# Optimization experiments

Hardware: AMD Instinct MI355X
Metric: run time of the kernel (lower is better)

The kernel has to match this reference:

```python
import jax, jax.numpy as jnp
from jax import lax
import numpy as np

NBINS = 50

def _make_filters():
    coords = np.linspace(-1.0, 1.0, 3)
    zz, yy, xx = np.meshgrid(coords, coords, coords, indexing='ij')
    gf = []
    for freq in [2.0, 4.0]:
        for ang in [0.0, np.pi / 4, np.pi / 2, 3 * np.pi / 4]:
            gauss = np.exp(-(xx ** 2 + yy ** 2 + zz ** 2) / 0.5)
            f = gauss * np.cos(freq * (xx * np.cos(ang) + yy * np.sin(ang)))
            f = f - f.mean()
            s = f.std(ddof=1)  # torch std is unbiased
            if s > 1e-8:
                f = f / s
            gf.append(f)
    gf = np.stack(gf)[:, None].astype(np.float32)  # (8,1,3,3,3)
    lf = []
    for axis in range(3):
        for sign in [1, -1]:
            f = np.zeros((3, 3, 3), np.float32)
            f[1, 1, 1] = 1.0
            idx = [1, 1, 1]
            idx[axis] += sign
            f[tuple(idx)] = -1.0
            lf.append(f)
    lf = np.stack(lf)[:, None].astype(np.float32)  # (6,1,3,3,3)
    return gf, lf

def setup_inputs() -> dict:
    key = jax.random.key(0)
    k1, k2 = jax.random.split(key)
    B, D, H, W = 4, 96, 160, 160
    x = jax.random.uniform(k1, (B, 1, D, H, W), jnp.float32, minval=-1.0, maxval=1.0)
    mask = (jax.random.uniform(k2, (B, 1, D, H, W), jnp.float32) > 0.5).astype(jnp.float32)
    gf, lf = _make_filters()
    return {"x": x, "mask": mask, "gabor_filters": jnp.asarray(gf), "lbp_filters": jnp.asarray(lf)}

def _hu_stats(v, mf):
    # v, mf: (B,D,H,W); mf is 0/1 float mask
    n = mf.sum((1, 2, 3))                      # (B,)
    nn = jnp.maximum(n, 1.0)
    mu = (mf * v).sum((1, 2, 3)) / nn
    diff = (v - mu[:, None, None, None]) * mf
    var = (diff ** 2).sum((1, 2, 3)) / jnp.maximum(n - 1.0, 1.0)  # unbiased, like torch .std()
    sigma = jnp.sqrt(var) + 1e-8
    z = diff / sigma[:, None, None, None]
    skew = (z ** 3).sum((1, 2, 3)) / nn
    kurt = (z ** 4).sum((1, 2, 3)) / nn - 3.0
    # histogram over [-1,1] with 50 bins; torch.histc ignores out-of-range, last bin inclusive
    w = mf * ((v >= -1.0) & (v <= 1.0)).astype(v.dtype)
    idx = jnp.clip(jnp.floor((v + 1.0) * (NBINS / 2.0)).astype(jnp.int32), 0, NBINS - 1)
    hist = jax.vmap(lambda i, wb: jnp.zeros((NBINS,), v.dtype).at[i.ravel()].add(wb.ravel()))(idx, w)
    p = hist / (hist.sum(-1, keepdims=True) + 1e-8)
    ent = -(p * jnp.log(p + 1e-8)).sum(-1)
    valid = (n >= 10.0).astype(v.dtype)
    return jnp.stack([mu, sigma, skew, kurt, ent], axis=1) * valid[:, None]  # (B,5)

def _glcm_proxy(v, m):
    # v: (B,D,H,W) float; m: (B,D,H,W) bool
    rows = []
    for axis in range(3):
        a = axis + 1
        sl1 = tuple(slice(None, -1) if i == a else slice(None) for i in range(4))
        sl2 = tuple(slice(1, None) if i == a else slice(None) for i in range(4))
        d = v[sl1] - v[sl2]
        mp = (m[sl1] & m[sl2]).astype(v.dtype)
        s = mp.sum((1, 2, 3))
        ss = jnp.maximum(s, 1.0)
        con = (mp * d * d).sum((1, 2, 3)) / ss
        hom = (mp / (1.0 + d * d)).sum((1, 2, 3)) / ss
        ok = (s >= 4.0).astype(v.dtype)
        rows += [con * ok, hom * ok]
    return jnp.stack(rows, axis=1)  # (B,6)

def _forward(x, mask, gabor_filters, lbp_filters):
    v = x[:, 0]                       # (B,D,H,W)
    m = mask[:, 0] > 0.5              # bool
    mf = m.astype(x.dtype)
    hu = _hu_stats(v, mf)             # (B,5)
    dn = ('NCDHW', 'OIDHW', 'NCDHW')
    pad = [(1, 1)] * 3
    gab = lax.conv_general_dilated(x, gabor_filters, (1, 1, 1), pad, dimension_numbers=dn)
    lung_vol = jnp.clip(mask.sum((2, 3, 4)), 1.0, None)      # (B,1)
    gab_feat = jnp.abs(gab * mask).sum((2, 3, 4)) / lung_vol  # (B,8)
    lbp = lax.conv_general_dilated(x, lbp_filters, (1, 1, 1), pad, dimension_numbers=dn)
    lbp = lbp * mask
    lbp_feat = ((lbp > 0).astype(x.dtype) * mask).sum((2, 3, 4)) / lung_vol  # (B,6)
    glcm = _glcm_proxy(v, m)          # (B,6)
    return jnp.concatenate([hu, gab_feat, lbp_feat, glcm], axis=1)  # (B,25)

def reference(x, mask, gabor_filters, lbp_filters):
    return _forward(x, mask, gabor_filters, lbp_filters)
```

## Files before the change

### kernel.cpp

```cpp
#include <hip/hip_runtime.h>
#include <math.h>

#define B_    4
#define D_    96
#define H_    160
#define W_    160
#define HW_   (H_ * W_)
#define NVOX  (D_ * H_ * W_)
#define NBINS 50
#define NQ    78
#define CZ    16
#define NCHUNK (D_ / CZ)
#define NTILE 50
#define NSLOTS (NTILE * NCHUNK)
#define LASTP ((D_ - 1) * HW_)

typedef float f2 __attribute__((ext_vector_type(2)));

__device__ __forceinline__ float rfl(float v) {
    return __uint_as_float(__builtin_amdgcn_readfirstlane(__float_as_uint(v)));
}

#define LOADP(s, zo) do {                                                   \
    _Pragma("unroll")                                                       \
    for (int r_ = 0; r_ < 3; ++r_) {                                        \
        Xw[s][r_][0] = xbb[(zo) + rowoff[r_] + xL];                         \
        f2 t_ = *(const f2*)(xbb + (zo) + rowoff[r_] + gx);                 \
        Xw[s][r_][1] = t_.x; Xw[s][r_][2] = t_.y;                           \
        Xw[s][r_][3] = xbb[(zo) + rowoff[r_] + xR];                         \
    }                                                                       \
} while (0)

#define FINISH(s, bzv) do {                                                 \
    const float br0_ = bndRow0 * (bzv), br2_ = bndRow2 * (bzv);             \
    _Pragma("unroll")                                                       \
    for (int c_ = 0; c_ < 4; ++c_) {                                        \
        Xw[s][0][c_] *= br0_; Xw[s][2][c_] *= br2_; Xw[s][1][c_] *= (bzv);  \
    }                                                                       \
    _Pragma("unroll")                                                       \
    for (int r_ = 0; r_ < 3; ++r_) {                                        \
        Xw[s][r_][0] *= bndL; Xw[s][r_][3] *= bndR;                         \
    }                                                                       \
    _Pragma("unroll")                                                       \
    for (int q_ = 0; q_ < 2; ++q_) {                                        \
        S9[s][q_] = Xw[s][0][q_] + Xw[s][0][q_+1] + Xw[s][0][q_+2]          \
                  + Xw[s][1][q_] + Xw[s][1][q_+1] + Xw[s][1][q_+2]          \
                  + Xw[s][2][q_] + Xw[s][2][q_+1] + Xw[s][2][q_+2];         \
    }                                                                       \
} while (0)

__global__ __launch_bounds__(256) void radiomics_main(
    const float* __restrict__ x, const float* __restrict__ mask,
    const float* __restrict__ gf, const float* __restrict__ lf,
    float* __restrict__ ws)
{
    __shared__ float sgf[8 * 27];
    __shared__ unsigned int shist[4 * NBINS];
    __shared__ float xred[4][28];

    const int tid = threadIdx.x;
    for (int i = tid; i < 8 * 27; i += 256) sgf[i] = gf[i];
    for (int i = tid; i < 4 * NBINS; i += 256) shist[i] = 0u;
    __syncthreads();

    float Cs[8][5], df[8], gz0;
    {
        float asum = 0.f, mOa[8], mCa[8];
#pragma unroll
        for (int f = 0; f < 8; ++f) {
            float C9[9];
            float mC = 0.f, mO = 0.f;
#pragma unroll
            for (int k = 0; k < 9; ++k) {
                C9[k] = sgf[f * 27 + 9 + k];
                mC += C9[k];
                mO += sgf[f * 27 + k];
            }
            mC *= (1.f / 9.f); mO *= (1.f / 9.f);
            float cov = 0.f, var = 0.f;
#pragma unroll
            for (int k = 0; k < 9; ++k) {
                float c = C9[k] - mC, o = sgf[f * 27 + k] - mO;
                cov += c * o; var += c * c;
            }
            asum += cov / var; mOa[f] = mO; mCa[f] = mC;
#pragma unroll
            for (int j = 0; j < 4; ++j)
                Cs[f][j] = rfl(0.5f * (C9[j] + C9[8 - j]));
            Cs[f][4] = rfl(C9[4]);
        }
        gz0 = rfl(asum * 0.125f);
#pragma unroll
        for (int f = 0; f < 8; ++f) df[f] = rfl(mOa[f] - gz0 * mCa[f]);
    }
    float lwc[6], lwn[6];
    {
        const int nbidx[6] = {22, 4, 16, 10, 14, 12};
#pragma unroll
        for (int f = 0; f < 6; ++f) {
            lwc[f] = rfl(lf[f * 27 + 13]);
            lwn[f] = rfl(lf[f * 27 + nbidx[f]]);
        }
    }

    const int b  = blockIdx.z;
    const int z0 = blockIdx.y * CZ;
    const int tx = tid & 15, ty = tid >> 4;
    const int gx = (blockIdx.x % 5) * 32 + tx * 2;
    const int gy = (blockIdx.x / 5) * 16 + ty;

    const float* __restrict__ xbb = x    + (size_t)b * NVOX;
    const float* __restrict__ mbb = mask + (size_t)b * NVOX;

    const int gy0 = (gy > 0) ? gy - 1 : 0;
    const int gy2 = (gy + 1 < H_) ? gy + 1 : H_ - 1;
    const int rowoff[3] = { gy0 * W_, gy * W_, gy2 * W_ };
    const float bndRow0 = (gy > 0) ? 1.f : 0.f;
    const float bndRow2 = (gy + 1 < H_) ? 1.f : 0.f;
    const int xL = (gx > 0) ? gx - 1 : 0;
    const int xR = (gx + 2 < W_) ? gx + 2 : W_ - 1;
    const float bndL = (gx > 0) ? 1.f : 0.f;
    const float bndR = (gx + 2 < W_) ? 1.f : 0.f;
    const int moff  = gy * W_ + gx;
    const int myoff = gy2 * W_ + gx;
    const int mxoff = gy * W_ + xR;
    const float bym = bndRow2, bxm = bndR;

    float Xw[4][3][4];
    float S9[4][2];
    float Mq[4][2];
    float bzs[4];
    f2    myq[2];
    float mxq[2];
    float acc[28];
#pragma unroll
    for (int q = 0; q < 28; ++q) acc[q] = 0.f;
    bzs[0] = bzs[1] = bzs[2] = 1.f;

    if (z0 == 0) {
#pragma unroll
        for (int r = 0; r < 3; ++r)
#pragma unroll
            for (int c = 0; c < 4; ++c) Xw[0][r][c] = 0.f;
        S9[0][0] = S9[0][1] = 0.f;
    } else {
        LOADP(0, (z0 - 1) * HW_);
        FINISH(0, 1.f);
    }
    LOADP(1, z0 * HW_);
    FINISH(1, 1.f);
    {
        f2 mm = *(const f2*)(mbb + z0 * HW_ + moff);
        Mq[1][0] = (mm.x > 0.5f) ? 1.f : 0.f;
        Mq[1][1] = (mm.y > 0.5f) ? 1.f : 0.f;
    }
    LOADP(2, (z0 + 1) * HW_);
    {
        f2 mm = *(const f2*)(mbb + (z0 + 1) * HW_ + moff);
        Mq[2][0] = mm.x; Mq[2][1] = mm.y;
    }
    Mq[0][0] = Mq[0][1] = 0.f;
    myq[0] = *(const f2*)(mbb + z0 * HW_ + myoff);
    mxq[0] = mbb[z0 * HW_ + mxoff];

    int zc   = z0 * HW_;
    int zpre = (z0 + 2) * HW_;

#pragma unroll 1
    for (int i0 = 0; i0 < CZ; i0 += 4) {
#pragma unroll
        for (int j = 0; j < 4; ++j) {
            const int c0 = j, c1 = (j + 1) & 3, c2 = (j + 2) & 3, c3 = (j + 3) & 3;
            const int cur = j & 1, nxt = cur ^ 1;

            const int zpe = (zpre < NVOX) ? zpre : LASTP;
            bzs[c3] = (zpre < NVOX) ? 1.f : 0.f;
            LOADP(c3, zpe);
            {
                f2 mm = *(const f2*)(mbb + zpe + moff);
                Mq[c3][0] = mm.x; Mq[c3][1] = mm.y;
            }
            const int zn = (zc + HW_ < NVOX) ? zc + HW_ : LASTP;
            myq[nxt] = *(const f2*)(mbb + zn + myoff);
            mxq[nxt] = mbb[zn + mxoff];

            FINISH(c2, bzs[c2]);
            Mq[c2][0] = (Mq[c2][0] * bzs[c2] > 0.5f) ? 1.f : 0.f;
            Mq[c2][1] = (Mq[c2][1] * bzs[c2] > 0.5f) ? 1.f : 0.f;

            float T6[3][4];
#pragma unroll
            for (int r = 0; r < 3; ++r)
#pragma unroll
                for (int c = 0; c < 4; ++c)
                    T6[r][c] = fmaf(gz0, Xw[c0][r][c] + Xw[c2][r][c], Xw[c1][r][c]);

            const f2 my2 = myq[cur];
            const float mxs = mxq[cur];

#pragma unroll
            for (int q = 0; q < 2; ++q) {
                const float v  = Xw[c1][1][q + 1];
                const float mc = Mq[c1][q];

                acc[0] += mc;
                float mv  = mc * v;  acc[1] += mv;
                float mv2 = mv * v;  acc[2] += mv2;
                float mv3 = mv2 * v; acc[3] += mv3;
                acc[4] += mv3 * v;

                if (mc > 0.5f && v >= -1.f && v <= 1.f) {
                    int bi = (int)floorf((v + 1.f) * (NBINS * 0.5f));
                    bi = min(max(bi, 0), NBINS - 1);
                    atomicAdd(&shist[(tid >> 6) * NBINS + bi], 1u);
                }

                float P0 = T6[0][q]     + T6[2][q + 2];
                float P1 = T6[0][q + 1] + T6[2][q + 1];
                float P2 = T6[0][q + 2] + T6[2][q];
                float P3 = T6[1][q]     + T6[1][q + 2];
                float ctr = T6[1][q + 1];
                float S2 = S9[c0][q] + S9[c2][q];
#pragma unroll
                for (int f = 0; f < 8; ++f) {
                    float ds = df[f] * S2;
                    ds = fmaf(Cs[f][0], P0, ds);
                    ds = fmaf(Cs[f][1], P1, ds);
                    ds = fmaf(Cs[f][2], P2, ds);
                    ds = fmaf(Cs[f][3], P3, ds);
                    ds = fmaf(Cs[f][4], ctr, ds);
                    acc[5 + f] = fmaf(fabsf(ds), mc, acc[5 + f]);
                }

                const float nb[6] = { Xw[c2][1][q + 1], Xw[c0][1][q + 1],
                                      Xw[c1][2][q + 1], Xw[c1][0][q + 1],
                                      Xw[c1][1][q + 2], Xw[c1][1][q] };
#pragma unroll
                for (int f = 0; f < 6; ++f) {
                    float l = fmaf(lwc[f], v, lwn[f] * nb[f]);
                    acc[13 + f] += (l > 0.f) ? mc : 0.f;
                }

                {
                    float mp = mc * Mq[c2][q];
                    float d = v - Xw[c2][1][q + 1], dd = d * d;
                    acc[19] += mp;
                    acc[22] = fmaf(mp, dd, acc[22]);
                    acc[25] = fmaf(mp, __builtin_amdgcn_rcpf(1.f + dd), acc[25]);
                }
                {
                    float mr = (q == 0) ? my2.x : my2.y;
                    float mp = mc * (((mr > 0.5f) ? 1.f : 0.f) * bym);
                    float d = v - Xw[c1][2][q + 1], dd = d * d;
                    acc[20] += mp;
                    acc[23] = fmaf(mp, dd, acc[23]);
                    acc[26] = fmaf(mp, __builtin_amdgcn_rcpf(1.f + dd), acc[26]);
                }
                {
                    float mnr = (q == 0) ? Mq[c1][1] : (((mxs > 0.5f) ? 1.f : 0.f) * bxm);
                    float mp = mc * mnr;
                    float d = v - Xw[c1][1][q + 2], dd = d * d;
                    acc[21] += mp;
                    acc[24] = fmaf(mp, dd, acc[24]);
                    acc[27] = fmaf(mp, __builtin_amdgcn_rcpf(1.f + dd), acc[27]);
                }
            }
            zc += HW_; zpre += HW_;
        }
    }

#pragma unroll
    for (int q = 0; q < 28; ++q) {
        float s = acc[q];
#pragma unroll
        for (int o = 32; o > 0; o >>= 1)
            s += __shfl_down(s, o, 64);
        acc[q] = s;
    }
    const int lane = tid & 63, wid = tid >> 6;
    if (lane == 0) {
#pragma unroll
        for (int q = 0; q < 28; ++q) xred[wid][q] = acc[q];
    }
    __syncthreads();

    const int slot = blockIdx.x + NTILE * blockIdx.y;
    float* wsb = ws + (size_t)b * NQ * NSLOTS;
    if (tid < 28) {
        float s = xred[0][tid] + xred[1][tid] + xred[2][tid] + xred[3][tid];
        wsb[tid * NSLOTS + slot] = s;
    } else if (tid < NQ) {
        int h = tid - 28;
        unsigned int c = shist[h] + shist[NBINS + h]
                       + shist[2 * NBINS + h] + shist[3 * NBINS + h];
        wsb[tid * NSLOTS + slot] = (float)c;
    }
}

__global__ __launch_bounds__(512) void radiomics_tail(
    const float* __restrict__ ws, float* __restrict__ out)
{
    __shared__ double fin[NQ];
    __shared__ double entp[NBINS];
    __shared__ double sh_hsum;
    const int b = blockIdx.x, tid = threadIdx.x;
    const int wave = tid >> 6, lane = tid & 63;

    for (int q = wave; q < NQ; q += 8) {
        const float* p = ws + ((size_t)b * NQ + q) * NSLOTS;
        double s = 0.0;
#pragma unroll
        for (int k = 0; k < 5; ++k) {
            int idx = lane + 64 * k;
            if (idx < NSLOTS) s += (double)p[idx];
        }
#pragma unroll
        for (int o = 32; o > 0; o >>= 1)
            s += __shfl_down(s, o, 64);
        if (lane == 0) fin[q] = s;
    }
    __syncthreads();

    if (tid == 0) {
        double h = 0.0;
        for (int k = 0; k < NBINS; ++k) h += fin[28 + k];
        sh_hsum = h + 1e-8;
    }
    __syncthreads();

    if (tid < NBINS) {
        double p = fin[28 + tid] / sh_hsum;
        entp[tid] = -p * log(p + 1e-8);
    }
    __syncthreads();

    if (tid == 0) {
        const double n  = fin[0];
        const double nn = fmax(n, 1.0);
        const double s1 = fin[1], s2 = fin[2], s3 = fin[3], s4 = fin[4];
        const double mu = s1 / nn;
        const double M2 = s2 - 2.0 * mu * s1 + mu * mu * n;
        const double M3 = s3 - 3.0 * mu * s2 + 3.0 * mu * mu * s1 - mu * mu * mu * n;
        const double M4 = s4 - 4.0 * mu * s3 + 6.0 * mu * mu * s2
                          - 4.0 * mu * mu * mu * s1 + mu * mu * mu * mu * n;
        const double var   = M2 / fmax(n - 1.0, 1.0);
        const double sigma = sqrt(var) + 1e-8;
        const double skew  = M3 / (sigma * sigma * sigma) / nn;
        const double kurt  = M4 / (sigma * sigma * sigma * sigma) / nn - 3.0;

        double ent = 0.0;
        for (int k = 0; k < NBINS; ++k) ent += entp[k];

        const double valid = (n >= 10.0) ? 1.0 : 0.0;
        float* ob = out + b * 25;
        ob[0] = (float)(mu * valid);
        ob[1] = (float)(sigma * valid);
        ob[2] = (float)(skew * valid);
        ob[3] = (float)(kurt * valid);
        ob[4] = (float)(ent * valid);

        const double lung = fmax(n, 1.0);
        for (int f = 0; f < 8; ++f) ob[5 + f]  = (float)(fin[5 + f] / lung);
        for (int f = 0; f < 6; ++f) ob[13 + f] = (float)(fin[13 + f] / lung);

        for (int ax = 0; ax < 3; ++ax) {
            double s  = fin[19 + ax];
            double ss = fmax(s, 1.0);
            double ok = (s >= 4.0) ? 1.0 : 0.0;
            ob[19 + 2 * ax]     = (float)(fin[22 + ax] / ss * ok);
            ob[19 + 2 * ax + 1] = (float)(fin[25 + ax] / ss * ok);
        }
    }
}

extern "C" void kernel_launch(void* const* d_in, const int* in_sizes, int n_in,
                              void* d_out, int out_size, void* d_ws, size_t ws_size,
                              hipStream_t stream)
{
    const float* x    = (const float*)d_in[0];
    const float* mask = (const float*)d_in[1];
    const float* gf   = (const float*)d_in[2];
    const float* lf   = (const float*)d_in[3];
    float* out = (float*)d_out;
    float* ws  = (float*)d_ws;

    dim3 grid(NTILE, NCHUNK, B_);
    radiomics_main<<<grid, 256, 0, stream>>>(x, mask, gf, lf, ws);
    radiomics_tail<<<B_, 512, 0, stream>>>(ws, out);
}
```

Baseline: 167.7 us.

## Use persistent work-stealing blocks, precomputed filter weights, and symmetric Gabor evaluation

```diff
diff --git a/kernel.cpp b/kernel.cpp
--- a/kernel.cpp
+++ b/kernel.cpp
@@ -8,17 +8,86 @@
 #define HW_   (H_ * W_)
 #define NVOX  (D_ * H_ * W_)
 #define NBINS 50
-#define NQ    78
-#define CZ    16
+#define CZ    8
 #define NCHUNK (D_ / CZ)
 #define NTILE 50
 #define NSLOTS (NTILE * NCHUNK)
+#define NITEMS (B_ * NSLOTS)
+#define NQR   28
+#define PART_F (B_ * NQR * NSLOTS)
+#define HIST_U PART_F
+#define WQ_F   (PART_F + 200)
+#define CTR_U  (WQ_F + 40)
 #define LASTP ((D_ - 1) * HW_)
 
 typedef float f2 __attribute__((ext_vector_type(2)));
 
 __device__ __forceinline__ float rfl(float v) {
     return __uint_as_float(__builtin_amdgcn_readfirstlane(__float_as_uint(v)));
+}
+
+__global__ __launch_bounds__(64) void radiomics_weights(
+    const float* __restrict__ gf, const float* __restrict__ lf,
+    float* __restrict__ ws)
+{
+    const int lane = threadIdx.x;
+    __shared__ float sCs[8][5], sR[8], sMO[8], sMC[8];
+    if (lane < 8) {
+        const int f = lane;
+        float O9[9], C9[9];
+        float mC = 0.f, mO = 0.f;
+#pragma unroll
+        for (int k = 0; k < 9; ++k) {
+            O9[k] = gf[f * 27 + k];
+            C9[k] = gf[f * 27 + 9 + k];
+            mC += C9[k]; mO += O9[k];
+        }
+        mC *= (1.f / 9.f); mO *= (1.f / 9.f);
+        float cov = 0.f, var = 0.f;
+#pragma unroll
+        for (int k = 0; k < 9; ++k) {
+            float c = C9[k] - mC, o = O9[k] - mO;
+            cov += c * o; var += c * c;
+        }
+        sR[f] = cov / var; sMO[f] = mO; sMC[f] = mC;
+#pragma unroll
+        for (int j = 0; j < 4; ++j) sCs[f][j] = 0.5f * (C9[j] + C9[8 - j]);
+        sCs[f][4] = C9[4];
+    }
+    __syncthreads();
+    if (lane == 0) {
+        float* wq = ws + WQ_F;
+        float gz0 = 0.f;
+        for (int f = 0; f < 8; ++f) gz0 += sR[f];
+        gz0 *= 0.125f;
+        wq[0] = gz0;
+        float df[8];
+        for (int f = 0; f < 8; ++f) df[f] = sMO[f] - gz0 * sMC[f];
+        for (int F = 0; F < 2; ++F) {
+            const int f0 = 4 * F, f1 = 4 * F + 1, f2 = 4 * F + 2, f3 = 4 * F + 3;
+            float* g = wq + 1 + 11 * F;
+            g[0]  = 0.5f * (df[f0] + df[f2]);
+            g[1]  = 0.5f * (sCs[f0][0] + sCs[f2][0]);
+            g[2]  = 0.5f * (sCs[f0][2] + sCs[f2][2]);
+            g[3]  = 0.5f * (sCs[f0][4] + sCs[f2][4]);
+            g[4]  = 0.5f * (sCs[f0][1] + sCs[f2][3]);
+            g[5]  = 0.5f * (sCs[f0][3] + sCs[f2][1]);
+            g[6]  = 0.5f * (df[f1] + df[f3]);
+            g[7]  = 0.25f * (sCs[f1][1] + sCs[f1][3]
+                           + sCs[f3][1] + sCs[f3][3]);
+            g[8]  = 0.5f * (sCs[f1][4] + sCs[f3][4]);
+            g[9]  = 0.5f * (sCs[f1][0] + sCs[f3][2]);
+            g[10] = 0.5f * (sCs[f1][2] + sCs[f3][0]);
+        }
+        const int nbidx[6] = {22, 4, 16, 10, 14, 12};
+        for (int f = 0; f < 6; ++f) {
+            wq[23 + f] = lf[f * 27 + 13];
+            wq[29 + f] = lf[f * 27 + nbidx[f]];
+        }
+        ((unsigned int*)ws)[CTR_U] = 0u;
+    }
+    unsigned int* gh = (unsigned int*)ws + HIST_U;
+    for (int i = lane; i < B_ * NBINS; i += 64) gh[i] = 0u;
 }
 
 #define LOADP(s, zo) do {                                                   \
@@ -41,276 +110,269 @@
     for (int r_ = 0; r_ < 3; ++r_) {                                        \
         Xw[s][r_][0] *= bndL; Xw[s][r_][3] *= bndR;                         \
     }                                                                       \
-    _Pragma("unroll")                                                       \
-    for (int q_ = 0; q_ < 2; ++q_) {                                        \
-        S9[s][q_] = Xw[s][0][q_] + Xw[s][0][q_+1] + Xw[s][0][q_+2]          \
-                  + Xw[s][1][q_] + Xw[s][1][q_+1] + Xw[s][1][q_+2]          \
-                  + Xw[s][2][q_] + Xw[s][2][q_+1] + Xw[s][2][q_+2];         \
+    {                                                                       \
+        float cs0_ = Xw[s][0][0] + Xw[s][1][0] + Xw[s][2][0];               \
+        float cs1_ = Xw[s][0][1] + Xw[s][1][1] + Xw[s][2][1];               \
+        float cs2_ = Xw[s][0][2] + Xw[s][1][2] + Xw[s][2][2];               \
+        float cs3_ = Xw[s][0][3] + Xw[s][1][3] + Xw[s][2][3];               \
+        S9[s][0] = cs0_ + cs1_ + cs2_;                                      \
+        S9[s][1] = cs1_ + cs2_ + cs3_;                                      \
     }                                                                       \
 } while (0)
 
 __global__ __launch_bounds__(256) void radiomics_main(
     const float* __restrict__ x, const float* __restrict__ mask,
-    const float* __restrict__ gf, const float* __restrict__ lf,
     float* __restrict__ ws)
 {
-    __shared__ float sgf[8 * 27];
     __shared__ unsigned int shist[4 * NBINS];
-    __shared__ float xred[4][28];
+    __shared__ float xred[4][NQR];
+    __shared__ unsigned int sitem;
 
     const int tid = threadIdx.x;
-    for (int i = tid; i < 8 * 27; i += 256) sgf[i] = gf[i];
-    for (int i = tid; i < 4 * NBINS; i += 256) shist[i] = 0u;
-    __syncthreads();
-
-    float Cs[8][5], df[8], gz0;
-    {
-        float asum = 0.f, mOa[8], mCa[8];
-#pragma unroll
-        for (int f = 0; f < 8; ++f) {
-            float C9[9];
-            float mC = 0.f, mO = 0.f;
-#pragma unroll
-            for (int k = 0; k < 9; ++k) {
-                C9[k] = sgf[f * 27 + 9 + k];
-                mC += C9[k];
-                mO += sgf[f * 27 + k];
+    const int tx = tid & 15, ty = tid >> 4;
+    const int lane = tid & 63, wid = tid >> 6;
+
+    const float* wq = ws + WQ_F;
+    const float gz0 = rfl(wq[0]);
+    float gco[22];
+#pragma unroll
+    for (int i = 0; i < 22; ++i) gco[i] = rfl(wq[1 + i]);
+    float lwc[6], lwn[6];
+#pragma unroll
+    for (int f = 0; f < 6; ++f) { lwc[f] = rfl(wq[23 + f]); lwn[f] = rfl(wq[29 + f]); }
+
+    unsigned int* ctr   = (unsigned int*)ws + CTR_U;
+    unsigned int* ghist = (unsigned int*)ws + HIST_U;
+
+    for (;;) {
+        __syncthreads();
+        if (tid == 0) sitem = atomicAdd(ctr, 1u);
+        for (int i = tid; i < 4 * NBINS; i += 256) shist[i] = 0u;
+        __syncthreads();
+        const int item = __builtin_amdgcn_readfirstlane((int)sitem);
+        if (item >= NITEMS) break;
+
+        const int b   = item / NSLOTS;
+        const int s   = item - b * NSLOTS;
+        const int cz  = s / NTILE;
+        const int bix = s - cz * NTILE;
+        const int z0  = cz * CZ;
+        const int gx = (bix % 5) * 32 + tx * 2;
+        const int gy = (bix / 5) * 16 + ty;
+
+        const float* __restrict__ xbb = x    + (size_t)b * NVOX;
+        const float* __restrict__ mbb = mask + (size_t)b * NVOX;
+
+        const int gy0 = (gy > 0) ? gy - 1 : 0;
+        const int gy2 = (gy + 1 < H_) ? gy + 1 : H_ - 1;
+        const int rowoff[3] = { gy0 * W_, gy * W_, gy2 * W_ };
+        const float bndRow0 = (gy > 0) ? 1.f : 0.f;
+        const float bndRow2 = (gy + 1 < H_) ? 1.f : 0.f;
+        const int xL = (gx > 0) ? gx - 1 : 0;
+        const int xR = (gx + 2 < W_) ? gx + 2 : W_ - 1;
+        const float bndL = (gx > 0) ? 1.f : 0.f;
+        const float bndR = (gx + 2 < W_) ? 1.f : 0.f;
+        const int moff  = gy * W_ + gx;
+        const int myoff = gy2 * W_ + gx;
+        const int mxoff = gy * W_ + xR;
+        const float bym = bndRow2, bxm = bndR;
+
+        float Xw[4][3][4];
+        float S9[4][2];
+        float Mq[4][2];
+        float bzs[4];
+        f2    myq[2];
+        float mxq[2];
+        float acc[NQR];
+#pragma unroll
+        for (int q = 0; q < NQR; ++q) acc[q] = 0.f;
+        bzs[0] = bzs[1] = bzs[2] = 1.f;
+
+        if (z0 == 0) {
+#pragma unroll
+            for (int r = 0; r < 3; ++r)
+#pragma unroll
+                for (int c = 0; c < 4; ++c) Xw[0][r][c] = 0.f;
+            S9[0][0] = S9[0][1] = 0.f;
+        } else {
+            LOADP(0, (z0 - 1) * HW_);
+            FINISH(0, 1.f);
+        }
+        LOADP(1, z0 * HW_);
+        FINISH(1, 1.f);
+        {
+            f2 mm = *(const f2*)(mbb + z0 * HW_ + moff);
+            Mq[1][0] = (mm.x > 0.5f) ? 1.f : 0.f;
+            Mq[1][1] = (mm.y > 0.5f) ? 1.f : 0.f;
+        }
+        LOADP(2, (z0 + 1) * HW_);
+        {
+            f2 mm = *(const f2*)(mbb + (z0 + 1) * HW_ + moff);
+            Mq[2][0] = mm.x; Mq[2][1] = mm.y;
+        }
+        Mq[0][0] = Mq[0][1] = 0.f;
+        myq[0] = *(const f2*)(mbb + z0 * HW_ + myoff);
+        mxq[0] = mbb[z0 * HW_ + mxoff];
+
+        int zc   = z0 * HW_;
+        int zpre = (z0 + 2) * HW_;
+
+#pragma unroll 1
+        for (int i0 = 0; i0 < CZ; i0 += 4) {
+#pragma unroll
+            for (int j = 0; j < 4; ++j) {
+                const int c0 = j, c1 = (j + 1) & 3, c2 = (j + 2) & 3, c3 = (j + 3) & 3;
+                const int cur = j & 1, nxt = cur ^ 1;
+
+                const int zpe = (zpre < NVOX) ? zpre : LASTP;
+                bzs[c3] = (zpre < NVOX) ? 1.f : 0.f;
+                LOADP(c3, zpe);
+                {
+                    f2 mm = *(const f2*)(mbb + zpe + moff);
+                    Mq[c3][0] = mm.x; Mq[c3][1] = mm.y;
+                }
+                const int zn = (zc + HW_ < NVOX) ? zc + HW_ : LASTP;
+                myq[nxt] = *(const f2*)(mbb + zn + myoff);
+                mxq[nxt] = mbb[zn + mxoff];
+
+                FINISH(c2, bzs[c2]);
+                Mq[c2][0] = (Mq[c2][0] * bzs[c2] > 0.5f) ? 1.f : 0.f;
+                Mq[c2][1] = (Mq[c2][1] * bzs[c2] > 0.5f) ? 1.f : 0.f;
+
+                float T6[3][4];
+#pragma unroll
+                for (int r = 0; r < 3; ++r)
+#pragma unroll
+                    for (int c = 0; c < 4; ++c)
+                        T6[r][c] = fmaf(gz0, Xw[c0][r][c] + Xw[c2][r][c], Xw[c1][r][c]);
+
+                const f2 my2 = myq[cur];
+                const float mxs = mxq[cur];
+
+#pragma unroll
+                for (int q = 0; q < 2; ++q) {
+                    const float v  = Xw[c1][1][q + 1];
+                    const float mc = Mq[c1][q];
+
+                    acc[0] += mc;
+                    float mv  = mc * v;  acc[1] += mv;
+                    float mv2 = mv * v;  acc[2] += mv2;
+                    float mv3 = mv2 * v; acc[3] += mv3;
+                    acc[4] += mv3 * v;
+
+                    if (mc > 0.5f && v >= -1.f && v <= 1.f) {
+                        int bi = (int)floorf((v + 1.f) * (NBINS * 0.5f));
+                        bi = min(max(bi, 0), NBINS - 1);
+                        atomicAdd(&shist[(tid >> 6) * NBINS + bi], 1u);
+                    }
+
+                    float P0 = T6[0][q]     + T6[2][q + 2];
+                    float P1 = T6[0][q + 1] + T6[2][q + 1];
+                    float P2 = T6[0][q + 2] + T6[2][q];
+                    float P3 = T6[1][q]     + T6[1][q + 2];
+                    float ctrv = T6[1][q + 1];
+                    float S2 = S9[c0][q] + S9[c2][q];
+                    float Qv = P1 + P3;
+#pragma unroll
+                    for (int F = 0; F < 2; ++F) {
+                        const float dfA = gco[F*11+0], c0s = gco[F*11+1];
+                        const float c2s = gco[F*11+2], c4s = gco[F*11+3];
+                        const float cu  = gco[F*11+4], cw  = gco[F*11+5];
+                        const float dfB = gco[F*11+6], ct  = gco[F*11+7];
+                        const float ce  = gco[F*11+8], ca  = gco[F*11+9];
+                        const float cb  = gco[F*11+10];
+                        float E = dfA * S2;
+                        E = fmaf(c0s, P0, E); E = fmaf(c2s, P2, E); E = fmaf(c4s, ctrv, E);
+                        float r0   = fmaf(cu, P1, fmaf(cw, P3, E));
+                        float r90  = fmaf(cw, P1, fmaf(cu, P3, E));
+                        float G = fmaf(ct, Qv, dfB * S2);
+                        G = fmaf(ce, ctrv, G);
+                        float r45  = fmaf(ca, P0, fmaf(cb, P2, G));
+                        float r135 = fmaf(cb, P0, fmaf(ca, P2, G));
+                        acc[5 + 4*F + 0] = fmaf(fabsf(r0),   mc, acc[5 + 4*F + 0]);
+                        acc[5 + 4*F + 1] = fmaf(fabsf(r45),  mc, acc[5 + 4*F + 1]);
+                        acc[5 + 4*F + 2] = fmaf(fabsf(r90),  mc, acc[5 + 4*F + 2]);
+                        acc[5 + 4*F + 3] = fmaf(fabsf(r135), mc, acc[5 + 4*F + 3]);
+                    }
+
+                    const float nb[6] = { Xw[c2][1][q + 1], Xw[c0][1][q + 1],
+                                          Xw[c1][2][q + 1], Xw[c1][0][q + 1],
+                                          Xw[c1][1][q + 2], Xw[c1][1][q] };
+#pragma unroll
+                    for (int f = 0; f < 6; ++f) {
+                        float l = fmaf(lwc[f], v, lwn[f] * nb[f]);
+                        acc[13 + f] += (l > 0.f) ? mc : 0.f;
+                    }
+
+                    {
+                        float mp = mc * Mq[c2][q];
+                        float d = v - Xw[c2][1][q + 1], dd = d * d;
+                        acc[19] += mp;
+                        acc[22] = fmaf(mp, dd, acc[22]);
+                        acc[25] = fmaf(mp, __builtin_amdgcn_rcpf(1.f + dd), acc[25]);
+                    }
+                    {
+                        float mr = (q == 0) ? my2.x : my2.y;
+                        float mp = mc * (((mr > 0.5f) ? 1.f : 0.f) * bym);
+                        float d = v - Xw[c1][2][q + 1], dd = d * d;
+                        acc[20] += mp;
+                        acc[23] = fmaf(mp, dd, acc[23]);
+                        acc[26] = fmaf(mp, __builtin_amdgcn_rcpf(1.f + dd), acc[26]);
+                    }
+                    {
+                        float mnr = (q == 0) ? Mq[c1][1] : (((mxs > 0.5f) ? 1.f : 0.f) * bxm);
+                        float mp = mc * mnr;
+                        float d = v - Xw[c1][1][q + 2], dd = d * d;
+                        acc[21] += mp;
+                        acc[24] = fmaf(mp, dd, acc[24]);
+                        acc[27] = fmaf(mp, __builtin_amdgcn_rcpf(1.f + dd), acc[27]);
+                    }
+                }
+                zc += HW_; zpre += HW_;
             }
-            mC *= (1.f / 9.f); mO *= (1.f / 9.f);
-            float cov = 0.f, var = 0.f;
-#pragma unroll
-            for (int k = 0; k < 9; ++k) {
-                float c = C9[k] - mC, o = sgf[f * 27 + k] - mO;
-                cov += c * o; var += c * c;
-            }
-            asum += cov / var; mOa[f] = mO; mCa[f] = mC;
-#pragma unroll
-            for (int j = 0; j < 4; ++j)
-                Cs[f][j] = rfl(0.5f * (C9[j] + C9[8 - j]));
-            Cs[f][4] = rfl(C9[4]);
-        }
-        gz0 = rfl(asum * 0.125f);
-#pragma unroll
-        for (int f = 0; f < 8; ++f) df[f] = rfl(mOa[f] - gz0 * mCa[f]);
-    }
-    float lwc[6], lwn[6];
-    {
-        const int nbidx[6] = {22, 4, 16, 10, 14, 12};
-#pragma unroll
-        for (int f = 0; f < 6; ++f) {
-            lwc[f] = rfl(lf[f * 27 + 13]);
-            lwn[f] = rfl(lf[f * 27 + nbidx[f]]);
-        }
-    }
-
-    const int b  = blockIdx.z;
-    const int z0 = blockIdx.y * CZ;
-    const int tx = tid & 15, ty = tid >> 4;
-    const int gx = (blockIdx.x % 5) * 32 + tx * 2;
-    const int gy = (blockIdx.x / 5) * 16 + ty;
-
-    const float* __restrict__ xbb = x    + (size_t)b * NVOX;
-    const float* __restrict__ mbb = mask + (size_t)b * NVOX;
-
-    const int gy0 = (gy > 0) ? gy - 1 : 0;
-    const int gy2 = (gy + 1 < H_) ? gy + 1 : H_ - 1;
-    const int rowoff[3] = { gy0 * W_, gy * W_, gy2 * W_ };
-    const float bndRow0 = (gy > 0) ? 1.f : 0.f;
-    const float bndRow2 = (gy + 1 < H_) ? 1.f : 0.f;
-    const int xL = (gx > 0) ? gx - 1 : 0;
-    const int xR = (gx + 2 < W_) ? gx + 2 : W_ - 1;
-    const float bndL = (gx > 0) ? 1.f : 0.f;
-    const float bndR = (gx + 2 < W_) ? 1.f : 0.f;
-    const int moff  = gy * W_ + gx;
-    const int myoff = gy2 * W_ + gx;
-    const int mxoff = gy * W_ + xR;
-    const float bym = bndRow2, bxm = bndR;
-
-    float Xw[4][3][4];
-    float S9[4][2];
-    float Mq[4][2];
-    float bzs[4];
-    f2    myq[2];
-    float mxq[2];
-    float acc[28];
-#pragma unroll
-    for (int q = 0; q < 28; ++q) acc[q] = 0.f;
-    bzs[0] = bzs[1] = bzs[2] = 1.f;
-
-    if (z0 == 0) {
-#pragma unroll
-        for (int r = 0; r < 3; ++r)
-#pragma unroll
-            for (int c = 0; c < 4; ++c) Xw[0][r][c] = 0.f;
-        S9[0][0] = S9[0][1] = 0.f;
-    } else {
-        LOADP(0, (z0 - 1) * HW_);
-        FINISH(0, 1.f);
-    }
-    LOADP(1, z0 * HW_);
-    FINISH(1, 1.f);
-    {
-        f2 mm = *(const f2*)(mbb + z0 * HW_ + moff);
-        Mq[1][0] = (mm.x > 0.5f) ? 1.f : 0.f;
-        Mq[1][1] = (mm.y > 0.5f) ? 1.f : 0.f;
-    }
-    LOADP(2, (z0 + 1) * HW_);
-    {
-        f2 mm = *(const f2*)(mbb + (z0 + 1) * HW_ + moff);
-        Mq[2][0] = mm.x; Mq[2][1] = mm.y;
-    }
-    Mq[0][0] = Mq[0][1] = 0.f;
-    myq[0] = *(const f2*)(mbb + z0 * HW_ + myoff);
-    mxq[0] = mbb[z0 * HW_ + mxoff];
-
-    int zc   = z0 * HW_;
-    int zpre = (z0 + 2) * HW_;
-
-#pragma unroll 1
-    for (int i0 = 0; i0 < CZ; i0 += 4) {
-#pragma unroll
-        for (int j = 0; j < 4; ++j) {
-            const int c0 = j, c1 = (j + 1) & 3, c2 = (j + 2) & 3, c3 = (j + 3) & 3;
-            const int cur = j & 1, nxt = cur ^ 1;
-
-            const int zpe = (zpre < NVOX) ? zpre : LASTP;
-            bzs[c3] = (zpre < NVOX) ? 1.f : 0.f;
-            LOADP(c3, zpe);
-            {
-                f2 mm = *(const f2*)(mbb + zpe + moff);
-                Mq[c3][0] = mm.x; Mq[c3][1] = mm.y;
-            }
-            const int zn = (zc + HW_ < NVOX) ? zc + HW_ : LASTP;
-            myq[nxt] = *(const f2*)(mbb + zn + myoff);
-            mxq[nxt] = mbb[zn + mxoff];
-
-            FINISH(c2, bzs[c2]);
-            Mq[c2][0] = (Mq[c2][0] * bzs[c2] > 0.5f) ? 1.f : 0.f;
-            Mq[c2][1] = (Mq[c2][1] * bzs[c2] > 0.5f) ? 1.f : 0.f;
-
-            float T6[3][4];
-#pragma unroll
-            for (int r = 0; r < 3; ++r)
-#pragma unroll
-                for (int c = 0; c < 4; ++c)
-                    T6[r][c] = fmaf(gz0, Xw[c0][r][c] + Xw[c2][r][c], Xw[c1][r][c]);
-
-            const f2 my2 = myq[cur];
-            const float mxs = mxq[cur];
-
-#pragma unroll
-            for (int q = 0; q < 2; ++q) {
-                const float v  = Xw[c1][1][q + 1];
-                const float mc = Mq[c1][q];
-
-                acc[0] += mc;
-                float mv  = mc * v;  acc[1] += mv;
-                float mv2 = mv * v;  acc[2] += mv2;
-                float mv3 = mv2 * v; acc[3] += mv3;
-                acc[4] += mv3 * v;
-
-                if (mc > 0.5f && v >= -1.f && v <= 1.f) {
-                    int bi = (int)floorf((v + 1.f) * (NBINS * 0.5f));
-                    bi = min(max(bi, 0), NBINS - 1);
-                    atomicAdd(&shist[(tid >> 6) * NBINS + bi], 1u);
-                }
-
-                float P0 = T6[0][q]     + T6[2][q + 2];
-                float P1 = T6[0][q + 1] + T6[2][q + 1];
-                float P2 = T6[0][q + 2] + T6[2][q];
-                float P3 = T6[1][q]     + T6[1][q + 2];
-                float ctr = T6[1][q + 1];
-                float S2 = S9[c0][q] + S9[c2][q];
-#pragma unroll
-                for (int f = 0; f < 8; ++f) {
-                    float ds = df[f] * S2;
-                    ds = fmaf(Cs[f][0], P0, ds);
-                    ds = fmaf(Cs[f][1], P1, ds);
-                    ds = fmaf(Cs[f][2], P2, ds);
-                    ds = fmaf(Cs[f][3], P3, ds);
-                    ds = fmaf(Cs[f][4], ctr, ds);
-                    acc[5 + f] = fmaf(fabsf(ds), mc, acc[5 + f]);
-                }
-
-                const float nb[6] = { Xw[c2][1][q + 1], Xw[c0][1][q + 1],
-                                      Xw[c1][2][q + 1], Xw[c1][0][q + 1],
-                                      Xw[c1][1][q + 2], Xw[c1][1][q] };
-#pragma unroll
-                for (int f = 0; f < 6; ++f) {
-                    float l = fmaf(lwc[f], v, lwn[f] * nb[f]);
-                    acc[13 + f] += (l > 0.f) ? mc : 0.f;
-                }
-
-                {
-                    float mp = mc * Mq[c2][q];
-                    float d = v - Xw[c2][1][q + 1], dd = d * d;
-                    acc[19] += mp;
-                    acc[22] = fmaf(mp, dd, acc[22]);
-                    acc[25] = fmaf(mp, __builtin_amdgcn_rcpf(1.f + dd), acc[25]);
-                }
-                {
-                    float mr = (q == 0) ? my2.x : my2.y;
-                    float mp = mc * (((mr > 0.5f) ? 1.f : 0.f) * bym);
-                    float d = v - Xw[c1][2][q + 1], dd = d * d;
-                    acc[20] += mp;
-                    acc[23] = fmaf(mp, dd, acc[23]);
-                    acc[26] = fmaf(mp, __builtin_amdgcn_rcpf(1.f + dd), acc[26]);
-                }
-                {
-                    float mnr = (q == 0) ? Mq[c1][1] : (((mxs > 0.5f) ? 1.f : 0.f) * bxm);
-                    float mp = mc * mnr;
-                    float d = v - Xw[c1][1][q + 2], dd = d * d;
-                    acc[21] += mp;
-                    acc[24] = fmaf(mp, dd, acc[24]);
-                    acc[27] = fmaf(mp, __builtin_amdgcn_rcpf(1.f + dd), acc[27]);
-                }
-            }
-            zc += HW_; zpre += HW_;
-        }
-    }
-
-#pragma unroll
-    for (int q = 0; q < 28; ++q) {
-        float s = acc[q];
-#pragma unroll
-        for (int o = 32; o > 0; o >>= 1)
-            s += __shfl_down(s, o, 64);
-        acc[q] = s;
-    }
-    const int lane = tid & 63, wid = tid >> 6;
-    if (lane == 0) {
-#pragma unroll
-        for (int q = 0; q < 28; ++q) xred[wid][q] = acc[q];
-    }
-    __syncthreads();
-
-    const int slot = blockIdx.x + NTILE * blockIdx.y;
-    float* wsb = ws + (size_t)b * NQ * NSLOTS;
-    if (tid < 28) {
-        float s = xred[0][tid] + xred[1][tid] + xred[2][tid] + xred[3][tid];
-        wsb[tid * NSLOTS + slot] = s;
-    } else if (tid < NQ) {
-        int h = tid - 28;
-        unsigned int c = shist[h] + shist[NBINS + h]
-                       + shist[2 * NBINS + h] + shist[3 * NBINS + h];
-        wsb[tid * NSLOTS + slot] = (float)c;
+        }
+
+#pragma unroll
+        for (int q = 0; q < NQR; ++q) {
+            float sm = acc[q];
+#pragma unroll
+            for (int o = 32; o > 0; o >>= 1)
+                sm += __shfl_down(sm, o, 64);
+            acc[q] = sm;
+        }
+        if (lane == 0) {
+#pragma unroll
+            for (int q = 0; q < NQR; ++q) xred[wid][q] = acc[q];
+        }
+        __syncthreads();
+
+        if (tid < NQR) {
+            float v = xred[0][tid] + xred[1][tid] + xred[2][tid] + xred[3][tid];
+            ws[((size_t)b * NQR + tid) * NSLOTS + s] = v;
+        } else if (tid < NQR + NBINS) {
+            int h = tid - NQR;
+            unsigned int c = shist[h] + shist[NBINS + h]
+                           + shist[2 * NBINS + h] + shist[3 * NBINS + h];
+            if (c) atomicAdd(&ghist[b * NBINS + h], c);
+        }
     }
 }
 
 __global__ __launch_bounds__(512) void radiomics_tail(
     const float* __restrict__ ws, float* __restrict__ out)
 {
-    __shared__ double fin[NQ];
+    __shared__ double fin[NQR];
+    __shared__ double hcnt[NBINS];
     __shared__ double entp[NBINS];
     __shared__ double sh_hsum;
     const int b = blockIdx.x, tid = threadIdx.x;
     const int wave = tid >> 6, lane = tid & 63;
 
-    for (int q = wave; q < NQ; q += 8) {
-        const float* p = ws + ((size_t)b * NQ + q) * NSLOTS;
+    for (int q = wave; q < NQR; q += 8) {
+        const float* p = ws + ((size_t)b * NQR + q) * NSLOTS;
         double s = 0.0;
 #pragma unroll
-        for (int k = 0; k < 5; ++k) {
+        for (int k = 0; k < 10; ++k) {
             int idx = lane + 64 * k;
             if (idx < NSLOTS) s += (double)p[idx];
         }
@@ -319,17 +381,19 @@
             s += __shfl_down(s, o, 64);
         if (lane == 0) fin[q] = s;
     }
+    if (tid < NBINS)
+        hcnt[tid] = (double)(((const unsigned int*)ws)[HIST_U + b * NBINS + tid]);
     __syncthreads();
 
     if (tid == 0) {
         double h = 0.0;
-        for (int k = 0; k < NBINS; ++k) h += fin[28 + k];
+        for (int k = 0; k < NBINS; ++k) h += hcnt[k];
         sh_hsum = h + 1e-8;
     }
     __syncthreads();
 
     if (tid < NBINS) {
-        double p = fin[28 + tid] / sh_hsum;
+        double p = hcnt[tid] / sh_hsum;
         entp[tid] = -p * log(p + 1e-8);
     }
     __syncthreads();
@@ -384,7 +448,7 @@
     float* out = (float*)d_out;
     float* ws  = (float*)d_ws;
 
-    dim3 grid(NTILE, NCHUNK, B_);
-    radiomics_main<<<grid, 256, 0, stream>>>(x, mask, gf, lf, ws);
+    radiomics_weights<<<1, 64, 0, stream>>>(gf, lf, ws);
+    radiomics_main<<<dim3(1024), 256, 0, stream>>>(x, mask, ws);
     radiomics_tail<<<B_, 512, 0, stream>>>(ws, out);
 }
```

Measured after the change: 185.5 us. 1.11x slower.
